# Kernel optimization log

Hardware: AMD Instinct MI355X
Metric: run time of the kernel (lower is better)

## Reference

```python
import jax, jax.numpy as jnp
import numpy as np

TIME_STEPS = 100
NUM_NEURONS = 100
MIN_VALUE, MAX_VALUE = -1.0, 1.0
SIGMA0, SPIKE_RATE0 = 0.2, 100.0


def setup_inputs() -> dict:
    key = jax.random.key(0)
    k_x, = jax.random.split(key, 1)
    x = jax.random.normal(k_x, (64, 128), dtype=jnp.float32)  # [B, F]
    centers = jnp.linspace(MIN_VALUE, MAX_VALUE, NUM_NEURONS, dtype=jnp.float32)  # [N]
    log_sigma = jnp.asarray(np.log(SIGMA0), dtype=jnp.float32)
    log_max_rate = jnp.asarray(np.log(SPIKE_RATE0), dtype=jnp.float32)
    return {"x": x, "centers": centers, "log_sigma": log_sigma, "log_max_rate": log_max_rate}


def reference(x, centers, log_sigma, log_max_rate):
    # Gaussian tuning curves: response [B, F, N]
    sigma = jnp.exp(log_sigma)
    max_rate = jnp.exp(log_max_rate)
    diff = x[:, :, None] - centers[None, None, :]
    response = jnp.exp(-(diff * diff) / (2.0 * sigma * sigma))
    firing_rates = response * max_rate / 1000.0  # per-ms Bernoulli prob
    # One fused draw of all T timesteps instead of a per-step loop.
    u = jax.random.uniform(jax.random.key(1),
                           (*firing_rates.shape, TIME_STEPS), dtype=jnp.float32)
    spikes = (u < firing_rates[..., None]).astype(jnp.float32)  # [B, F, N, T]
    return spikes
```

## Files before the change

kernel.cpp:

```cpp
#include <hip/hip_runtime.h>
#include <math.h>


#define TOTAL_N 81920000u
#define ELEMS_PER_BLOCK 2048u

__device__ __forceinline__ void tfr(uint32_t& x0, uint32_t& x1, uint32_t r) {
  x0 += x1;
  x1 = __builtin_rotateleft32(x1, r) ^ x0;
}

__device__ __forceinline__ uint32_t threefry_xor(uint32_t p) {
  const uint32_t ks2 = 0x1BD11BDBu;
  const uint32_t x1i = p + 1u;
  uint32_t x0 = x1i;
  uint32_t x1 = __builtin_rotateleft32(x1i, 13) ^ x0;
  tfr(x0, x1, 15); tfr(x0, x1, 26); tfr(x0, x1, 6);
  x0 += 1u;  x1 += ks2 + 1u;
  tfr(x0, x1, 17); tfr(x0, x1, 29); tfr(x0, x1, 16); tfr(x0, x1, 24);
  x0 += ks2; x1 += 2u;
  tfr(x0, x1, 13); tfr(x0, x1, 15); tfr(x0, x1, 26); tfr(x0, x1, 6);
   x1 += 4u;
  tfr(x0, x1, 17); tfr(x0, x1, 29); tfr(x0, x1, 16); tfr(x0, x1, 24);
  x0 += 1u;  x1 += ks2 + 4u;
  tfr(x0, x1, 13); tfr(x0, x1, 15); tfr(x0, x1, 26); tfr(x0, x1, 6);
  x0 += ks2; x1 += 5u;
  return x0 ^ x1;
}

__global__ __launch_bounds__(256) void popenc_kernel(
    const float* __restrict__ x,
    const float* __restrict__ centers,
    const float* __restrict__ log_sigma,
    const float* __restrict__ log_max_rate,
    float* __restrict__ out) {
  __shared__ uint32_t sK9[22];

  const uint32_t B0 = blockIdx.x * ELEMS_PER_BLOCK;
  const uint32_t rowFirst = B0 / 100u;
  const uint32_t rowLast  = (B0 + ELEMS_PER_BLOCK - 1u) / 100u;
  const uint32_t nRows    = rowLast - rowFirst + 1u;
  const uint32_t tid = threadIdx.x;

  if (tid < nRows) {
    const uint32_t row = rowFirst + tid;
    const float sigma = (float)exp((double)log_sigma[0]);
    const float mrate = (float)exp((double)log_max_rate[0]);
    const float s2    = __fmul_rn(__fmul_rn(2.0f, sigma), sigma);
    const uint32_t xidx = row / 100u;
    const uint32_t n    = row % 100u;
    const float d    = __fsub_rn(x[xidx], centers[n]);
    const float num  = __fmul_rn(d, d);
    const float arg  = __fdiv_rn(-num, s2);
    const float resp = (float)exp((double)arg);
    const float fr   = __fdiv_rn(__fmul_rn(resp, mrate), 1000.0f);
    const float rs   = __fmul_rn(fr, 8388608.0f);
    sK9[tid] = ((uint32_t)ceilf(rs)) << 9;
  }
  __syncthreads();

  const uint32_t pA = B0 + tid * 4u;
  const uint32_t pB = pA + 1024u;
  const uint32_t KA9 = sK9[(pA / 100u) - rowFirst];
  const uint32_t KB9 = sK9[(pB / 100u) - rowFirst];

  float4 qa, qb;
  qa.x = (threefry_xor(pA + 0u) < KA9) ? 1.0f : 0.0f;
  qa.y = (threefry_xor(pA + 1u) < KA9) ? 1.0f : 0.0f;
  qa.z = (threefry_xor(pA + 2u) < KA9) ? 1.0f : 0.0f;
  qa.w = (threefry_xor(pA + 3u) < KA9) ? 1.0f : 0.0f;
  qb.x = (threefry_xor(pB + 0u) < KB9) ? 1.0f : 0.0f;
  qb.y = (threefry_xor(pB + 1u) < KB9) ? 1.0f : 0.0f;
  qb.z = (threefry_xor(pB + 2u) < KB9) ? 1.0f : 0.0f;
  qb.w = (threefry_xor(pB + 3u) < KB9) ? 1.0f : 0.0f;

  *reinterpret_cast<float4*>(out + pA) = qa;
  *reinterpret_cast<float4*>(out + pB) = qb;
}

extern "C" void kernel_launch(void* const* d_in, const int* in_sizes, int n_in,
                              void* d_out, int out_size, void* d_ws, size_t ws_size,
                              hipStream_t stream) {
  const float* x            = (const float*)d_in[0];
  const float* centers      = (const float*)d_in[1];
  const float* log_sigma    = (const float*)d_in[2];
  const float* log_max_rate = (const float*)d_in[3];
  float* out = (float*)d_out;

  const uint32_t nblocks = TOTAL_N / ELEMS_PER_BLOCK;
  popenc_kernel<<<dim3(nblocks), dim3(256), 0, stream>>>(
      x, centers, log_sigma, log_max_rate, out);
}
```

Before: 155.6 us.

## Split threshold table into separate kernel and double elements per block

Adds a pre-pass kernel that writes the per-row spike thresholds to workspace, so the main kernel reads them from global memory instead of computing them inside every block and waiting at a barrier. Each thread now handles 16 outputs instead of 8. The threefry round code is rewritten with the key injections folded into the adds. The extra launch and the workspace round-trip cost something, and when no workspace is available a fallback single-kernel path with the larger per-block work is used.

Result: faster. 151.1 us (-2.9%).

```diff
diff --git a/kernel.cpp b/kernel.cpp
--- a/kernel.cpp
+++ b/kernel.cpp
@@ -3,79 +3,124 @@
 
 
 #define TOTAL_N 81920000u
-#define ELEMS_PER_BLOCK 2048u
+#define NROWS   819200u
+#define ELEMS_PER_BLOCK 4096u
 
-__device__ __forceinline__ void tfr(uint32_t& x0, uint32_t& x1, uint32_t r) {
-  x0 += x1;
-  x1 = __builtin_rotateleft32(x1, r) ^ x0;
+__device__ __forceinline__ uint32_t rotl(uint32_t x, uint32_t d) {
+  return __builtin_rotateleft32(x, d);
 }
 
 __device__ __forceinline__ uint32_t threefry_xor(uint32_t p) {
   const uint32_t ks2 = 0x1BD11BDBu;
-  const uint32_t x1i = p + 1u;
-  uint32_t x0 = x1i;
-  uint32_t x1 = __builtin_rotateleft32(x1i, 13) ^ x0;
-  tfr(x0, x1, 15); tfr(x0, x1, 26); tfr(x0, x1, 6);
-  x0 += 1u;  x1 += ks2 + 1u;
-  tfr(x0, x1, 17); tfr(x0, x1, 29); tfr(x0, x1, 16); tfr(x0, x1, 24);
-  x0 += ks2; x1 += 2u;
-  tfr(x0, x1, 13); tfr(x0, x1, 15); tfr(x0, x1, 26); tfr(x0, x1, 6);
-   x1 += 4u;
-  tfr(x0, x1, 17); tfr(x0, x1, 29); tfr(x0, x1, 16); tfr(x0, x1, 24);
-  x0 += 1u;  x1 += ks2 + 4u;
-  tfr(x0, x1, 13); tfr(x0, x1, 15); tfr(x0, x1, 26); tfr(x0, x1, 6);
-  x0 += ks2; x1 += 5u;
-  return x0 ^ x1;
+  const uint32_t a = p + 1u;
+  uint32_t x0 = a;
+  uint32_t x1 = rotl(a, 13) ^ x0;
+  x0 += x1; x1 = rotl(x1, 15) ^ x0;
+  x0 += x1; x1 = rotl(x1, 26) ^ x0;
+  x0 += x1; x1 = rotl(x1, 6)  ^ x0;
+  x1 += ks2 + 1u;
+  x0 = x0 + 1u + x1;
+  x1 = rotl(x1, 17) ^ x0;
+  x0 += x1; x1 = rotl(x1, 29) ^ x0;
+  x0 += x1; x1 = rotl(x1, 16) ^ x0;
+  x0 += x1; x1 = rotl(x1, 24) ^ x0;
+  x1 += 2u;
+  x0 = x0 + ks2 + x1;
+  x1 = rotl(x1, 13) ^ x0;
+  x0 += x1; x1 = rotl(x1, 15) ^ x0;
+  x0 += x1; x1 = rotl(x1, 26) ^ x0;
+  x0 += x1; x1 = rotl(x1, 6)  ^ x0;
+  x1 += 4u;
+  x0 += x1;
+  x1 = rotl(x1, 17) ^ x0;
+  x0 += x1; x1 = rotl(x1, 29) ^ x0;
+  x0 += x1; x1 = rotl(x1, 16) ^ x0;
+  x0 += x1; x1 = rotl(x1, 24) ^ x0;
+  x1 += ks2 + 4u;
+  x0 = x0 + 1u + x1;
+  x1 = rotl(x1, 13) ^ x0;
+  x0 += x1; x1 = rotl(x1, 15) ^ x0;
+  x0 += x1; x1 = rotl(x1, 26) ^ x0;
+  x0 += x1; x1 = rotl(x1, 6)  ^ x0;
+  return (x0 + ks2) ^ (x1 + 5u);
 }
 
-__global__ __launch_bounds__(256) void popenc_kernel(
+__global__ __launch_bounds__(256) void build_k9(
+    const float* __restrict__ x,
+    const float* __restrict__ centers,
+    const float* __restrict__ log_sigma,
+    const float* __restrict__ log_max_rate,
+    uint32_t* __restrict__ K9) {
+  const uint32_t row = blockIdx.x * 256u + threadIdx.x;
+  if (row >= NROWS) return;
+  const float sigma = (float)exp((double)log_sigma[0]);
+  const float mrate = (float)exp((double)log_max_rate[0]);
+  const float s2    = __fmul_rn(__fmul_rn(2.0f, sigma), sigma);
+  const uint32_t xidx = row / 100u;
+  const uint32_t n    = row % 100u;
+  const float d    = __fsub_rn(x[xidx], centers[n]);
+  const float num  = __fmul_rn(d, d);
+  const float arg  = __fdiv_rn(-num, s2);
+  const float resp = (float)exp((double)arg);
+  const float fr   = __fdiv_rn(__fmul_rn(resp, mrate), 1000.0f);
+  const float rs   = __fmul_rn(fr, 8388608.0f);
+  K9[row] = ((uint32_t)ceilf(rs)) << 9;
+}
+
+__global__ __launch_bounds__(256) void popenc_tab(
+    const uint32_t* __restrict__ K9,
+    float* __restrict__ out) {
+  const uint32_t t4 = blockIdx.x * ELEMS_PER_BLOCK + threadIdx.x * 4u;
+  uint32_t k[4];
+#pragma unroll
+  for (uint32_t q = 0; q < 4u; ++q) k[q] = K9[(t4 + q * 1024u) / 100u];
+#pragma unroll
+  for (uint32_t q = 0; q < 4u; ++q) {
+    const uint32_t p = t4 + q * 1024u;
+    float4 o;
+    o.x = (threefry_xor(p + 0u) < k[q]) ? 1.0f : 0.0f;
+    o.y = (threefry_xor(p + 1u) < k[q]) ? 1.0f : 0.0f;
+    o.z = (threefry_xor(p + 2u) < k[q]) ? 1.0f : 0.0f;
+    o.w = (threefry_xor(p + 3u) < k[q]) ? 1.0f : 0.0f;
+    *reinterpret_cast<float4*>(out + p) = o;
+  }
+}
+
+__global__ __launch_bounds__(256) void popenc_fb(
     const float* __restrict__ x,
     const float* __restrict__ centers,
     const float* __restrict__ log_sigma,
     const float* __restrict__ log_max_rate,
     float* __restrict__ out) {
-  __shared__ uint32_t sK9[22];
-
+  __shared__ uint32_t sK9[44];
   const uint32_t B0 = blockIdx.x * ELEMS_PER_BLOCK;
   const uint32_t rowFirst = B0 / 100u;
-  const uint32_t rowLast  = (B0 + ELEMS_PER_BLOCK - 1u) / 100u;
-  const uint32_t nRows    = rowLast - rowFirst + 1u;
+  const uint32_t nRows = (B0 + ELEMS_PER_BLOCK - 1u) / 100u - rowFirst + 1u;
   const uint32_t tid = threadIdx.x;
-
   if (tid < nRows) {
     const uint32_t row = rowFirst + tid;
     const float sigma = (float)exp((double)log_sigma[0]);
     const float mrate = (float)exp((double)log_max_rate[0]);
     const float s2    = __fmul_rn(__fmul_rn(2.0f, sigma), sigma);
-    const uint32_t xidx = row / 100u;
-    const uint32_t n    = row % 100u;
-    const float d    = __fsub_rn(x[xidx], centers[n]);
-    const float num  = __fmul_rn(d, d);
-    const float arg  = __fdiv_rn(-num, s2);
-    const float resp = (float)exp((double)arg);
-    const float fr   = __fdiv_rn(__fmul_rn(resp, mrate), 1000.0f);
-    const float rs   = __fmul_rn(fr, 8388608.0f);
-    sK9[tid] = ((uint32_t)ceilf(rs)) << 9;
+    const float d     = __fsub_rn(x[row / 100u], centers[row % 100u]);
+    const float arg   = __fdiv_rn(-__fmul_rn(d, d), s2);
+    const float resp  = (float)exp((double)arg);
+    const float fr    = __fdiv_rn(__fmul_rn(resp, mrate), 1000.0f);
+    sK9[tid] = ((uint32_t)ceilf(__fmul_rn(fr, 8388608.0f))) << 9;
   }
   __syncthreads();
-
-  const uint32_t pA = B0 + tid * 4u;
-  const uint32_t pB = pA + 1024u;
-  const uint32_t KA9 = sK9[(pA / 100u) - rowFirst];
-  const uint32_t KB9 = sK9[(pB / 100u) - rowFirst];
-
-  float4 qa, qb;
-  qa.x = (threefry_xor(pA + 0u) < KA9) ? 1.0f : 0.0f;
-  qa.y = (threefry_xor(pA + 1u) < KA9) ? 1.0f : 0.0f;
-  qa.z = (threefry_xor(pA + 2u) < KA9) ? 1.0f : 0.0f;
-  qa.w = (threefry_xor(pA + 3u) < KA9) ? 1.0f : 0.0f;
-  qb.x = (threefry_xor(pB + 0u) < KB9) ? 1.0f : 0.0f;
-  qb.y = (threefry_xor(pB + 1u) < KB9) ? 1.0f : 0.0f;
-  qb.z = (threefry_xor(pB + 2u) < KB9) ? 1.0f : 0.0f;
-  qb.w = (threefry_xor(pB + 3u) < KB9) ? 1.0f : 0.0f;
-
-  *reinterpret_cast<float4*>(out + pA) = qa;
-  *reinterpret_cast<float4*>(out + pB) = qb;
+  const uint32_t t4 = B0 + tid * 4u;
+#pragma unroll
+  for (uint32_t q = 0; q < 4u; ++q) {
+    const uint32_t p = t4 + q * 1024u;
+    const uint32_t kq = sK9[(p / 100u) - rowFirst];
+    float4 o;
+    o.x = (threefry_xor(p + 0u) < kq) ? 1.0f : 0.0f;
+    o.y = (threefry_xor(p + 1u) < kq) ? 1.0f : 0.0f;
+    o.z = (threefry_xor(p + 2u) < kq) ? 1.0f : 0.0f;
+    o.w = (threefry_xor(p + 3u) < kq) ? 1.0f : 0.0f;
+    *reinterpret_cast<float4*>(out + p) = o;
+  }
 }
 
 extern "C" void kernel_launch(void* const* d_in, const int* in_sizes, int n_in,
@@ -88,6 +133,13 @@
   float* out = (float*)d_out;
 
   const uint32_t nblocks = TOTAL_N / ELEMS_PER_BLOCK;
-  popenc_kernel<<<dim3(nblocks), dim3(256), 0, stream>>>(
-      x, centers, log_sigma, log_max_rate, out);
+  if (d_ws != nullptr && ws_size >= (size_t)NROWS * 4u) {
+    uint32_t* K9 = (uint32_t*)d_ws;
+    build_k9<<<dim3(NROWS / 256u), dim3(256), 0, stream>>>(
+        x, centers, log_sigma, log_max_rate, K9);
+    popenc_tab<<<dim3(nblocks), dim3(256), 0, stream>>>(K9, out);
+  } else {
+    popenc_fb<<<dim3(nblocks), dim3(256), 0, stream>>>(
+        x, centers, log_sigma, log_max_rate, out);
+  }
 }
```
